# Kernel tuning notes

Hardware: AMD Instinct MI355X
Metric: run time of the kernel (lower is better)

## Reference

```python
import jax, jax.numpy as jnp
import numpy as np

D_MODEL = 2048
D_STATE = 64
D_HEAD = 64
EXPAND = 2
CHUNK = 256
D_INNER = EXPAND * D_MODEL          # 4096
N_HEADS = D_INNER // D_HEAD          # 64
PARAM_DIM = 1 + 2 * D_STATE          # 129


def setup_inputs() -> dict:
    key = jax.random.key(0)
    k0, k1, k2, k3 = jax.random.split(key, 4)
    x = jax.random.normal(k0, (1, 4096, D_MODEL), jnp.float32)
    w_in = jax.random.normal(k1, (2 * D_INNER, D_MODEL), jnp.float32) * 0.02
    w_param = jax.random.normal(k2, (N_HEADS * PARAM_DIM, D_MODEL), jnp.float32) * 0.02
    w_out = jax.random.normal(k3, (D_MODEL, D_INNER), jnp.float32) * 0.02
    return {"x": x, "w_in": w_in, "w_param": w_param, "w_out": w_out}


def _ssd(a, Bm, Cm, X, Q):
    # a: (nb, l), Bm/Cm: (nb, l, ds), X: (nb, l, dh). Mamba-2 SSD chunked scan.
    nb, l = a.shape
    ds = Bm.shape[-1]
    dh = X.shape[-1]
    nc = l // Q
    la = jnp.log(a).reshape(nb, nc, Q)
    cs = jnp.cumsum(la, axis=-1)                      # cumulative log-decay within chunk
    Bc = Bm.reshape(nb, nc, Q, ds)
    Cc = Cm.reshape(nb, nc, Q, ds)
    Xc = X.reshape(nb, nc, Q, dh)
    # intra-chunk (attention-like dual): L[i,j] = prod_{r=j+1..i} a_r, j<=i
    tri = jnp.tril(jnp.ones((Q, Q), bool))
    L = jnp.where(tri, jnp.exp(cs[..., :, None] - cs[..., None, :]), 0.0)
    scores = jnp.einsum('znid,znjd->znij', Cc, Bc) * L
    y_diag = jnp.einsum('znij,znjh->znih', scores, Xc)
    # per-chunk state contribution: sum_j decay_to_end[j] * B_j^T x_j -> (nb,nc,ds,dh)
    decay_states = jnp.exp(cs[..., -1:] - cs)
    states = jnp.einsum('znj,znjd,znjh->zndh', decay_states, Bc, Xc)
    A_chunk = jnp.exp(cs[..., -1])                    # total decay per chunk (nb, nc)
    def step(S, inp):
        Ac, st = inp
        S_prev = S
        return Ac[:, None, None] * S + st, S_prev
    S0 = jnp.zeros((nb, ds, dh), a.dtype)
    _, S_prev = jax.lax.scan(step, S0, (A_chunk.T, jnp.moveaxis(states, 1, 0)))
    S_prev = jnp.moveaxis(S_prev, 0, 1)               # state entering each chunk (nb,nc,ds,dh)
    y_inter = jnp.einsum('znid,zndh,zni->znih', Cc, S_prev, jnp.exp(cs))
    return (y_diag + y_inter).reshape(nb, l, dh)


def reference(x, w_in, w_param, w_out):
    b, l, _ = x.shape
    xr = x @ w_in.T                                   # (b, l, 2*d_inner)
    inp, res = xr[..., :D_INNER], xr[..., D_INNER:]
    params = (x @ w_param.T).reshape(b, l, N_HEADS, PARAM_DIM)
    dt = jax.nn.softplus(params[..., 0])
    a = jnp.exp(-dt)                                  # (b, l, n_heads)
    Bp = params[..., 1:1 + D_STATE]
    Cp = params[..., 1 + D_STATE:]
    nb = b * N_HEADS
    # NOTE: raw row-major reshapes, mirroring the torch source exactly
    y = _ssd(a.reshape(nb, l),
             Bp.reshape(nb, l, D_STATE),
             Cp.reshape(nb, l, D_STATE),
             inp.reshape(nb, l, D_HEAD),
             CHUNK)
    y = y.reshape(b, l, D_INNER)
    out = y * jax.nn.silu(res)
    return out @ w_out.T
```

## Files before the change

kernel.cpp:

```cpp
#include <hip/hip_runtime.h>
#include <math.h>

#define Q 256

typedef unsigned short u16;
typedef unsigned int u32;
typedef __attribute__((ext_vector_type(8))) short short8;
typedef __attribute__((ext_vector_type(4))) float f32x4;

__device__ __forceinline__ float bf2f(u32 u){
  union { float f; u32 i; } v; v.i = u << 16; return v.f;
}
__device__ __forceinline__ u16 f2bf(float f){
  union { float f; u32 i; } v; v.f = f;
  u32 r = (v.i + 0x7FFFu + ((v.i >> 16) & 1u)) >> 16;
  return (u16)r;
}
__device__ __forceinline__ float softplusf(float x){
  return x > 20.f ? x : log1pf(expf(x));
}
__device__ __forceinline__ float siluf(float x){
  return x / (1.f + expf(-x));
}

__device__ __forceinline__ void gload_lds16(const void* g, const void* l){
  __builtin_amdgcn_global_load_lds(
    (const __attribute__((address_space(1))) void*)(uintptr_t)g,
    (__attribute__((address_space(3))) void*)(u32)(uintptr_t)l,
    16, 0, 0);
}

__device__ __forceinline__ u32 swz_off(int row, int col2){
  return (u32)(row*128 + (col2 ^ ((row & 7) << 4)));
}
__device__ __forceinline__ short8 frag_ld(const u16* buf, int row, int kk, int lk){
  return *(const short8*)((const char*)buf + row*128 + (((kk*4 + lk) ^ (row & 7)) << 4));
}

__global__ __launch_bounds__(256) void cast_all(const float* __restrict__ x,
    const float* __restrict__ w_in, const float* __restrict__ w_param,
    const float* __restrict__ w_out, u16* __restrict__ xb,
    u16* __restrict__ w_in_b, u16* __restrict__ w_param_b, u16* __restrict__ w_out_b)
{
  const size_t g = (size_t)blockIdx.x * 256 + threadIdx.x;
  const float* src; u16* dst; size_t off;
  if (g < 2097152)        { src = x;       dst = xb;        off = g; }
  else if (g < 6291456)   { src = w_in;    dst = w_in_b;    off = g - 2097152; }
  else if (g < 10518528)  { src = w_param; dst = w_param_b; off = g - 6291456; }
  else                    { src = w_out;   dst = w_out_b;   off = g - 10518528; }
  const float4 v = *(const float4*)(src + off*4);
  ushort4 o;
  o.x = f2bf(v.x); o.y = f2bf(v.y); o.z = f2bf(v.z); o.w = f2bf(v.w);
  *(ushort4*)(dst + off*4) = o;
}

#define T256_STAGE(s_) \
  _Pragma("unroll") for (int q = 0; q < 3; q++) \
    gload_lds16(sptr[q] + (s_)*32, lds + (((s_)&1)*24576) + (q*512 + tid)*16);

#define T256_CORE(A_, B_, K_, NTN_) \
  __shared__ char lds[49152]; \
  const int tid = threadIdx.x; \
  const int nwg = gridDim.x, bid = blockIdx.x; \
  const int wg = (bid & 7) * (nwg >> 3) + (bid >> 3); \
  const int m0 = (wg / (NTN_)) * 128, n0 = (wg % (NTN_)) * 256; \
  const int w = tid >> 6, l = tid & 63; \
  const int wr = w >> 2, wc = w & 3; \
  const int lr = l & 15, lk = l >> 4; \
  const u16* sptr[3]; \
  _Pragma("unroll") for (int q = 0; q < 3; q++) { \
    const int c = q*512 + tid; \
    const int r = c >> 3; \
    const int lg = (c & 7) ^ (r & 7); \
    const int lrow2 = 2*r + (lg >> 2); \
    const int kc = lg & 3; \
    sptr[q] = (lrow2 < 128) ? ((A_) + (size_t)(m0 + lrow2)*(K_) + kc*8) \
                            : ((B_) + (size_t)(n0 + (lrow2 - 128))*(K_) + kc*8); \
  } \
  const int arow0 = wr*64 + lr; \
  const int abrow = arow0 >> 1; \
  const int abase = abrow*128 + ((((arow0 & 1)*4 + lk) ^ (abrow & 7)) << 4); \
  const int brow0 = 64 + ((wc*64 + lr) >> 1); \
  const int bbase = brow0*128 + ((((lr & 1)*4 + lk) ^ (brow0 & 7)) << 4); \
  f32x4 acc[4][4]; \
  { f32x4 z = {0.f,0.f,0.f,0.f}; \
    _Pragma("unroll") for (int m = 0; m < 4; m++) \
    _Pragma("unroll") for (int n = 0; n < 4; n++) acc[m][n] = z; } \
  T256_STAGE(0) \
  asm volatile("s_waitcnt vmcnt(0)" ::: "memory"); \
  __builtin_amdgcn_s_barrier(); \
  { const int NS = (K_)/32; \
    for (int s = 0; s < NS-1; ++s) { \
      const char* sb_ = lds + ((s & 1)*24576); \
      short8 aF[4], bF[4]; \
      T256_STAGE(s+1) \
      _Pragma("unroll") for (int m = 0; m < 4; m++) \
        aF[m] = *(const short8*)(sb_ + abase + m*1024); \
      _Pragma("unroll") for (int n = 0; n < 4; n++) \
        bF[n] = *(const short8*)(sb_ + bbase + n*1024); \
      __builtin_amdgcn_s_setprio(1); \
      _Pragma("unroll") for (int m = 0; m < 4; m++) \
      _Pragma("unroll") for (int n = 0; n < 4; n++) \
        acc[m][n] = __builtin_amdgcn_mfma_f32_16x16x32_bf16(aF[m], bF[n], acc[m][n], 0, 0, 0); \
      __builtin_amdgcn_s_setprio(0); \
      asm volatile("s_waitcnt vmcnt(0)" ::: "memory"); \
      __builtin_amdgcn_s_barrier(); \
    } \
    { const char* sb_ = lds + (((K_)/32 - 1) & 1)*24576; \
      short8 aF[4], bF[4]; \
      _Pragma("unroll") for (int m = 0; m < 4; m++) \
        aF[m] = *(const short8*)(sb_ + abase + m*1024); \
      _Pragma("unroll") for (int n = 0; n < 4; n++) \
        bF[n] = *(const short8*)(sb_ + bbase + n*1024); \
      _Pragma("unroll") for (int m = 0; m < 4; m++) \
      _Pragma("unroll") for (int n = 0; n < 4; n++) \
        acc[m][n] = __builtin_amdgcn_mfma_f32_16x16x32_bf16(aF[m], bF[n], acc[m][n], 0, 0, 0); \
    } \
  }

__global__ void __launch_bounds__(512, 4) gemm_in256(const u16* __restrict__ A,
    const u16* __restrict__ B, u16* __restrict__ inp, u16* __restrict__ resb)
{
  T256_CORE(A, B, 2048, 32)
  #pragma unroll
  for (int m = 0; m < 4; m++)
    #pragma unroll
    for (int n = 0; n < 4; n++) {
      const int col = n0 + wc*64 + n*16 + lr;
      #pragma unroll
      for (int j = 0; j < 4; j++) {
        const int row = m0 + wr*64 + m*16 + lk*4 + j;
        const u16 v = f2bf(acc[m][n][j]);
        if (col < 4096) inp[(size_t)row*4096 + col] = v;
        else            resb[(size_t)row*4096 + (col - 4096)] = v;
      }
    }
}

__global__ void __launch_bounds__(512, 4) gemm_par256(const u16* __restrict__ A,
    const u16* __restrict__ B, float* __restrict__ dtb,
    u16* __restrict__ Bb, u16* __restrict__ Cb)
{
  T256_CORE(A, B, 2048, 33)
  #pragma unroll
  for (int m = 0; m < 4; m++)
    #pragma unroll
    for (int n = 0; n < 4; n++) {
      const int col = n0 + wc*64 + n*16 + lr;
      if (col < 8256) {
        const int h = col / 129, rr = col - h*129;
        #pragma unroll
        for (int j = 0; j < 4; j++) {
          const int row = m0 + wr*64 + m*16 + lk*4 + j;
          const float v = acc[m][n][j];
          if (rr == 0)      dtb[(size_t)row*64 + h] = v;
          else if (rr < 65) Bb[((size_t)row*64 + h)*64 + (rr-1)]  = f2bf(v);
          else              Cb[((size_t)row*64 + h)*64 + (rr-65)] = f2bf(v);
        }
      }
    }
}

__global__ void __launch_bounds__(512, 4) gemm_out256(const u16* __restrict__ A,
    const u16* __restrict__ B, float* __restrict__ C)
{
  T256_CORE(A, B, 4096, 8)
  #pragma unroll
  for (int m = 0; m < 4; m++)
    #pragma unroll
    for (int n = 0; n < 4; n++) {
      const int col = n0 + wc*64 + n*16 + lr;
      #pragma unroll
      for (int j = 0; j < 4; j++)
        C[(size_t)(m0 + wr*64 + m*16 + lk*4 + j)*2048 + col] = acc[m][n][j];
    }
}

__global__ __launch_bounds__(256) void ssd_phaseA(const float* __restrict__ dtb,
    const u16* __restrict__ Bb, const u16* __restrict__ inp,
    float* __restrict__ cs_g, float* __restrict__ achunk, float* __restrict__ states_t)
{
  const int g = blockIdx.x, tid = threadIdx.x;
  const int p = g * Q + tid;
  __shared__ float sc[Q];
  __shared__ u16 sBt[64*64];
  __shared__ u16 sXt[64*64];
  sc[tid] = -softplusf(dtb[p]);
  __syncthreads();
  for (int off = 1; off < Q; off <<= 1) {
    float v = (tid >= off) ? sc[tid - off] : 0.f;
    __syncthreads();
    if (tid >= off) sc[tid] += v;
    __syncthreads();
  }
  cs_g[p] = sc[tid];
  const float cl = sc[Q-1];
  if (tid == 0) achunk[g] = expf(cl);

  const int w = tid >> 6, l = tid & 63;
  const int lrow = l & 15, lk = l >> 4;
  const int tj = tid & 63, tcb = (tid >> 6) * 16;
  f32x4 acc[4];
  { f32x4 z = {0,0,0,0}; acc[0]=z; acc[1]=z; acc[2]=z; acc[3]=z; }

  for (int js = 0; js < 4; js++) {
    __syncthreads();
    {
      const int jc = js*64 + tj;
      const float wj = expf(cl - sc[jc]);
      const size_t prow = ((size_t)g*Q + jc) * 64;
      union { uint4 v; u16 s[8]; } b0, b1, x0, x1;
      b0.v = *(const uint4*)&Bb[prow + tcb];
      b1.v = *(const uint4*)&Bb[prow + tcb + 8];
      x0.v = *(const uint4*)&inp[prow + tcb];
      x1.v = *(const uint4*)&inp[prow + tcb + 8];
      #pragma unroll
      for (int q = 0; q < 8; q++) {
        const int r0 = tcb + q, r1 = tcb + 8 + q;
        *(u16*)((char*)sBt + swz_off(r0, 2*tj)) = f2bf(wj * bf2f((u32)b0.s[q]));
        *(u16*)((char*)sBt + swz_off(r1, 2*tj)) = f2bf(wj * bf2f((u32)b1.s[q]));
        *(u16*)((char*)sXt + swz_off(r0, 2*tj)) = x0.s[q];
        *(u16*)((char*)sXt + swz_off(r1, 2*tj)) = x1.s[q];
      }
    }
    __syncthreads();
    short8 aX0 = frag_ld(sXt, w*16 + lrow, 0, lk);
    short8 aX1 = frag_ld(sXt, w*16 + lrow, 1, lk);
    #pragma unroll
    for (int n = 0; n < 4; n++) {
      short8 b0 = frag_ld(sBt, n*16 + lrow, 0, lk);
      short8 b1 = frag_ld(sBt, n*16 + lrow, 1, lk);
      acc[n] = __builtin_amdgcn_mfma_f32_16x16x32_bf16(aX0, b0, acc[n], 0, 0, 0);
      acc[n] = __builtin_amdgcn_mfma_f32_16x16x32_bf16(aX1, b1, acc[n], 0, 0, 0);
    }
  }
  #pragma unroll
  for (int reg = 0; reg < 4; reg++) {
    const int d = w*16 + lk*4 + reg;
    #pragma unroll
    for (int n = 0; n < 4; n++)
      states_t[(size_t)g*4096 + d*64 + n*16 + lrow] = acc[n][reg];
  }
}

__global__ __launch_bounds__(256) void ssd_scan(float* __restrict__ states,
    const float* __restrict__ achunk)
{
  const int n = blockIdx.x, tid = threadIdx.x;
  float S[16];
  #pragma unroll
  for (int k = 0; k < 16; k++) S[k] = 0.f;
  for (int c = 0; c < 16; c++) {
    const int g = n*16 + c;
    const float A = achunk[g];
    #pragma unroll
    for (int k = 0; k < 16; k++) {
      const size_t e = (size_t)g * 4096 + tid + k*256;
      const float st = states[e];
      states[e] = S[k];
      S[k] = fmaf(A, S[k], st);
    }
  }
}

__global__ __launch_bounds__(256) void ssd_diag(const u16* __restrict__ Bb,
    const u16* __restrict__ Cb, const u16* __restrict__ inp,
    const float* __restrict__ cs_g, const float* __restrict__ states_t,
    const u16* __restrict__ resb, u16* __restrict__ yb)
{
  const int g = blockIdx.y, it = blockIdx.x, tid = threadIdx.x;
  const int w = tid >> 6, l = tid & 63;
  const int lrow = l & 15, lk = l >> 4;
  const int p_base = g * Q;
  __shared__ u16 sC[64*64];
  __shared__ u16 sB[64*64];
  __shared__ u16 sX[64*64];
  __shared__ u16 sP[64*64];
  __shared__ float csi[64], csj[64];

  const int r = tid >> 2, c0 = (tid & 3) << 4;
  {
    const size_t prow = (size_t)(p_base + it*64 + r) * 64;
    uint4 v0 = *(const uint4*)&Cb[prow + c0];
    uint4 v1 = *(const uint4*)&Cb[prow + c0 + 8];
    *(uint4*)((char*)sC + swz_off(r, c0*2))      = v0;
    *(uint4*)((char*)sC + swz_off(r, c0*2 + 16)) = v1;
    if (tid < 64) csi[tid] = cs_g[p_base + it*64 + tid];
  }
  const int i0 = w * 16;
  const int xj = tid & 63, xdb = (tid >> 6) * 16;
  f32x4 accY[4];
  { f32x4 z = {0,0,0,0}; accY[0]=z; accY[1]=z; accY[2]=z; accY[3]=z; }

  for (int jt = 0; jt <= it; jt++) {
    __syncthreads();
    {
      const size_t prow = (size_t)(p_base + jt*64 + r) * 64;
      uint4 v0 = *(const uint4*)&Bb[prow + c0];
      uint4 v1 = *(const uint4*)&Bb[prow + c0 + 8];
      *(uint4*)((char*)sB + swz_off(r, c0*2))      = v0;
      *(uint4*)((char*)sB + swz_off(r, c0*2 + 16)) = v1;
      if (tid < 64) csj[tid] = cs_g[p_base + jt*64 + tid];
    }
    {
      const size_t prow = (size_t)(p_base + jt*64 + xj) * 64;
      union { uint4 v; u16 s[8]; } x0, x1;
      x0.v = *(const uint4*)&inp[prow + xdb];
      x1.v = *(const uint4*)&inp[prow + xdb + 8];
      #pragma unroll
      for (int q = 0; q < 8; q++) {
        *(u16*)((char*)sX + swz_off(xdb + q,     2*xj)) = x0.s[q];
        *(u16*)((char*)sX + swz_off(xdb + 8 + q, 2*xj)) = x1.s[q];
      }
    }
    __syncthreads();
    f32x4 sAcc[4];
    { f32x4 z = {0,0,0,0}; sAcc[0]=z; sAcc[1]=z; sAcc[2]=z; sAcc[3]=z; }
    {
      short8 aC0 = frag_ld(sC, i0 + lrow, 0, lk);
      short8 aC1 = frag_ld(sC, i0 + lrow, 1, lk);
      #pragma unroll
      for (int n = 0; n < 4; n++) {
        short8 b0 = frag_ld(sB, n*16 + lrow, 0, lk);
        short8 b1 = frag_ld(sB, n*16 + lrow, 1, lk);
        sAcc[n] = __builtin_amdgcn_mfma_f32_16x16x32_bf16(aC0, b0, sAcc[n], 0, 0, 0);
        sAcc[n] = __builtin_amdgcn_mfma_f32_16x16x32_bf16(aC1, b1, sAcc[n], 0, 0, 0);
      }
    }
    const bool full = (jt < it);
    #pragma unroll
    for (int n = 0; n < 4; n++) {
      const int j_l = n*16 + lrow;
      const float cj = csj[j_l];
      #pragma unroll
      for (int reg = 0; reg < 4; reg++) {
        const int i_l = i0 + lk*4 + reg;
        float s = 0.f;
        if (full || j_l <= i_l) s = sAcc[n][reg] * expf(csi[i_l] - cj);
        *(u16*)((char*)sP + swz_off(i_l, n*32 + 2*lrow)) = f2bf(s);
      }
    }
    {
      short8 aP0 = frag_ld(sP, i0 + lrow, 0, lk);
      short8 aP1 = frag_ld(sP, i0 + lrow, 1, lk);
      #pragma unroll
      for (int n = 0; n < 4; n++) {
        short8 x0f = frag_ld(sX, n*16 + lrow, 0, lk);
        short8 x1f = frag_ld(sX, n*16 + lrow, 1, lk);
        accY[n] = __builtin_amdgcn_mfma_f32_16x16x32_bf16(aP0, x0f, accY[n], 0, 0, 0);
        accY[n] = __builtin_amdgcn_mfma_f32_16x16x32_bf16(aP1, x1f, accY[n], 0, 0, 0);
      }
    }
  }
  __syncthreads();
  {
    const int d = tid & 63, sb = (tid >> 6) * 16;
    const float* srow = &states_t[(size_t)g*4096 + d*64 + sb];
    float4 f0 = *(const float4*)(srow);
    float4 f1 = *(const float4*)(srow + 4);
    float4 f2 = *(const float4*)(srow + 8);
    float4 f3 = *(const float4*)(srow + 12);
    union { uint4 v; u16 s[8]; } o0, o1;
    o0.s[0]=f2bf(f0.x); o0.s[1]=f2bf(f0.y); o0.s[2]=f2bf(f0.z); o0.s[3]=f2bf(f0.w);
    o0.s[4]=f2bf(f1.x); o0.s[5]=f2bf(f1.y); o0.s[6]=f2bf(f1.z); o0.s[7]=f2bf(f1.w);
    o1.s[0]=f2bf(f2.x); o1.s[1]=f2bf(f2.y); o1.s[2]=f2bf(f2.z); o1.s[3]=f2bf(f2.w);
    o1.s[4]=f2bf(f3.x); o1.s[5]=f2bf(f3.y); o1.s[6]=f2bf(f3.z); o1.s[7]=f2bf(f3.w);
    *(uint4*)((char*)sB + swz_off(d, sb*2))      = o0.v;
    *(uint4*)((char*)sB + swz_off(d, sb*2 + 16)) = o1.v;
  }
  __syncthreads();
  f32x4 accI[4];
  { f32x4 z = {0,0,0,0}; accI[0]=z; accI[1]=z; accI[2]=z; accI[3]=z; }
  {
    short8 aC0 = frag_ld(sC, i0 + lrow, 0, lk);
    short8 aC1 = frag_ld(sC, i0 + lrow, 1, lk);
    #pragma unroll
    for (int n = 0; n < 4; n++) {
      short8 s0 = frag_ld(sB, n*16 + lrow, 0, lk);
      short8 s1 = frag_ld(sB, n*16 + lrow, 1, lk);
      accI[n] = __builtin_amdgcn_mfma_f32_16x16x32_bf16(aC0, s0, accI[n], 0, 0, 0);
      accI[n] = __builtin_amdgcn_mfma_f32_16x16x32_bf16(aC1, s1, accI[n], 0, 0, 0);
    }
  }
  #pragma unroll
  for (int reg = 0; reg < 4; reg++) {
    const int i_l = i0 + lk*4 + reg;
    const float ei = expf(csi[i_l]);
    const size_t prow = (size_t)(p_base + it*64 + i_l) * 64;
    #pragma unroll
    for (int n = 0; n < 4; n++) {
      const int d = n*16 + lrow;
      const float yv = accY[n][reg] + ei * accI[n][reg];
      const float rv = bf2f((u32)resb[prow + d]);
      yb[prow + d] = f2bf(yv * siluf(rv));
    }
  }
}

extern "C" void kernel_launch(void* const* d_in, const int* in_sizes, int n_in,
                              void* d_out, int out_size, void* d_ws, size_t ws_size,
                              hipStream_t stream)
{
  const float* x       = (const float*)d_in[0];
  const float* w_in    = (const float*)d_in[1];
  const float* w_param = (const float*)d_in[2];
  const float* w_out   = (const float*)d_in[3];
  float* out = (float*)d_out;
  char* ws = (char*)d_ws;

  float* states    = (float*)(ws);
  u16*   xb        = (u16*)  (ws);
  u16*   yb        = (u16*)  (ws + 0x1000000ull);
  u16*   w_in_b    = (u16*)  (ws + 0x1000000ull);
  u16*   w_param_b = (u16*)  (ws + 0x3000000ull);
  u16*   w_out_b   = (u16*)  (ws + 0x5100000ull);
  u16*   inp       = (u16*)  (ws + 0x6100000ull);
  u16*   resb      = (u16*)  (ws + 0x8100000ull);
  u16*   Bb        = (u16*)  (ws + 0xA100000ull);
  u16*   Cb        = (u16*)  (ws + 0xC100000ull);
  float* dtb       = (float*)(ws + 0xE100000ull);
  float* cs        = (float*)(ws + 0xE200000ull);
  float* achunk    = (float*)(ws + 0xE300000ull);

  cast_all<<<49280, 256, 0, stream>>>(x, w_in, w_param, w_out,
                                      xb, w_in_b, w_param_b, w_out_b);

  gemm_in256 <<<1024, 512, 0, stream>>>(xb, w_in_b, inp, resb);
  gemm_par256<<<1056, 512, 0, stream>>>(xb, w_param_b, dtb, Bb, Cb);
  ssd_phaseA<<<1024, 256, 0, stream>>>(dtb, Bb, inp, cs, achunk, states);
  ssd_scan<<<64, 256, 0, stream>>>(states, achunk);
  ssd_diag<<<dim3(4, 1024), 256, 0, stream>>>(Bb, Cb, inp, cs, states, resb, yb);
  gemm_out256<<<256, 512, 0, stream>>>(yb, w_out_b, out);
}
```

Measured before the change: 561.9 us.

## Merge input and param GEMMs into one launch; retile output GEMM to 128x128

The input and parameter projection GEMMs now share one grid, and each workgroup selects its weight matrix and epilogue by index. This removes a launch boundary and the tail idle time between the two kernels. The output GEMM uses 128x128 tiles with a 64-deep K step, doubling the workgroup count to fill more CUs. The smaller tiles reuse less data per load, and the larger LDS footprint can lower occupancy.

```diff
diff --git a/kernel.cpp b/kernel.cpp
--- a/kernel.cpp
+++ b/kernel.cpp
@@ -58,12 +58,8 @@
   _Pragma("unroll") for (int q = 0; q < 3; q++) \
     gload_lds16(sptr[q] + (s_)*32, lds + (((s_)&1)*24576) + (q*512 + tid)*16);
 
-#define T256_CORE(A_, B_, K_, NTN_) \
+#define T256_BODY(A_, B_, K_) \
   __shared__ char lds[49152]; \
-  const int tid = threadIdx.x; \
-  const int nwg = gridDim.x, bid = blockIdx.x; \
-  const int wg = (bid & 7) * (nwg >> 3) + (bid >> 3); \
-  const int m0 = (wg / (NTN_)) * 128, n0 = (wg % (NTN_)) * 256; \
   const int w = tid >> 6, l = tid & 63; \
   const int wr = w >> 2, wc = w & 3; \
   const int lr = l & 15, lk = l >> 4; \
@@ -118,58 +114,145 @@
     } \
   }
 
-__global__ void __launch_bounds__(512, 4) gemm_in256(const u16* __restrict__ A,
-    const u16* __restrict__ B, u16* __restrict__ inp, u16* __restrict__ resb)
-{
-  T256_CORE(A, B, 2048, 32)
-  #pragma unroll
-  for (int m = 0; m < 4; m++)
-    #pragma unroll
-    for (int n = 0; n < 4; n++) {
-      const int col = n0 + wc*64 + n*16 + lr;
-      #pragma unroll
-      for (int j = 0; j < 4; j++) {
-        const int row = m0 + wr*64 + m*16 + lk*4 + j;
-        const u16 v = f2bf(acc[m][n][j]);
-        if (col < 4096) inp[(size_t)row*4096 + col] = v;
-        else            resb[(size_t)row*4096 + (col - 4096)] = v;
-      }
-    }
-}
-
-__global__ void __launch_bounds__(512, 4) gemm_par256(const u16* __restrict__ A,
-    const u16* __restrict__ B, float* __restrict__ dtb,
-    u16* __restrict__ Bb, u16* __restrict__ Cb)
-{
-  T256_CORE(A, B, 2048, 33)
-  #pragma unroll
-  for (int m = 0; m < 4; m++)
-    #pragma unroll
-    for (int n = 0; n < 4; n++) {
-      const int col = n0 + wc*64 + n*16 + lr;
-      if (col < 8256) {
-        const int h = col / 129, rr = col - h*129;
+__global__ void __launch_bounds__(512, 4) gemm_inpar(const u16* __restrict__ A,
+    const u16* __restrict__ Bin, const u16* __restrict__ Bpar,
+    u16* __restrict__ inp, u16* __restrict__ resb,
+    float* __restrict__ dtb, u16* __restrict__ Bb, u16* __restrict__ Cb)
+{
+  const int tid = threadIdx.x;
+  const int nwg = gridDim.x, bid = blockIdx.x;
+  const int wg = (bid & 7) * (nwg >> 3) + (bid >> 3);
+  const bool isPar = (wg >= 1024);
+  int m0, n0;
+  const u16* Bmat;
+  if (!isPar) { Bmat = Bin;  m0 = (wg >> 5) * 128;        n0 = (wg & 31) * 256; }
+  else        { Bmat = Bpar; const int w2 = wg - 1024;
+                m0 = (w2 / 33) * 128;                      n0 = (w2 % 33) * 256; }
+  T256_BODY(A, Bmat, 2048)
+  if (!isPar) {
+    #pragma unroll
+    for (int m = 0; m < 4; m++)
+      #pragma unroll
+      for (int n = 0; n < 4; n++) {
+        const int col = n0 + wc*64 + n*16 + lr;
         #pragma unroll
         for (int j = 0; j < 4; j++) {
           const int row = m0 + wr*64 + m*16 + lk*4 + j;
-          const float v = acc[m][n][j];
-          if (rr == 0)      dtb[(size_t)row*64 + h] = v;
-          else if (rr < 65) Bb[((size_t)row*64 + h)*64 + (rr-1)]  = f2bf(v);
-          else              Cb[((size_t)row*64 + h)*64 + (rr-65)] = f2bf(v);
+          const u16 v = f2bf(acc[m][n][j]);
+          if (col < 4096) inp[(size_t)row*4096 + col] = v;
+          else            resb[(size_t)row*4096 + (col - 4096)] = v;
         }
       }
-    }
-}
-
-__global__ void __launch_bounds__(512, 4) gemm_out256(const u16* __restrict__ A,
+  } else {
+    #pragma unroll
+    for (int m = 0; m < 4; m++)
+      #pragma unroll
+      for (int n = 0; n < 4; n++) {
+        const int col = n0 + wc*64 + n*16 + lr;
+        if (col < 8256) {
+          const int h = col / 129, rr = col - h*129;
+          #pragma unroll
+          for (int j = 0; j < 4; j++) {
+            const int row = m0 + wr*64 + m*16 + lk*4 + j;
+            const float v = acc[m][n][j];
+            if (rr == 0)      dtb[(size_t)row*64 + h] = v;
+            else if (rr < 65) Bb[((size_t)row*64 + h)*64 + (rr-1)]  = f2bf(v);
+            else              Cb[((size_t)row*64 + h)*64 + (rr-65)] = f2bf(v);
+          }
+        }
+      }
+  }
+}
+
+#define O128_STAGE(s_) \
+  _Pragma("unroll") for (int q = 0; q < 4; q++) \
+    gload_lds16(sptr[q] + (s_)*64, lds + (((s_)&1)*32768) + (q*512 + tid)*16);
+
+__global__ void __launch_bounds__(512, 4) gemm_out64(const u16* __restrict__ A,
     const u16* __restrict__ B, float* __restrict__ C)
 {
-  T256_CORE(A, B, 4096, 8)
+  __shared__ char lds[65536];
+  const int tid = threadIdx.x;
+  const int nwg = gridDim.x, bid = blockIdx.x;
+  const int wg = (bid & 7) * (nwg >> 3) + (bid >> 3);
+  const int m0 = (wg >> 4) * 128, n0 = (wg & 15) * 128;
+  const int w = tid >> 6, l = tid & 63;
+  const int wr = w >> 2, wc = w & 3;
+  const int lr = l & 15, lk = l >> 4;
+  const u16* sptr[4];
+  #pragma unroll
+  for (int q = 0; q < 4; q++) {
+    const int c = q*512 + tid;
+    const int r = c >> 3;
+    const int jl = (c & 7) ^ (r & 7);
+    sptr[q] = (r < 128) ? (A + (size_t)(m0 + r)*4096 + jl*8)
+                        : (B + (size_t)(n0 + (r - 128))*4096 + jl*8);
+  }
+  const int ko0 = ((lk       ^ (lr & 7)) << 4);
+  const int ko1 = (((4 + lk) ^ (lr & 7)) << 4);
+  const int abase = (wr*64 + lr) * 128;
+  const int bbase = (128 + wc*32 + lr) * 128;
+  f32x4 acc[4][2];
+  { f32x4 z = {0.f,0.f,0.f,0.f};
+    #pragma unroll
+    for (int m = 0; m < 4; m++)
+      #pragma unroll
+      for (int n = 0; n < 2; n++) acc[m][n] = z; }
+  O128_STAGE(0)
+  asm volatile("s_waitcnt vmcnt(0)" ::: "memory");
+  __builtin_amdgcn_s_barrier();
+  for (int s = 0; s < 63; ++s) {
+    const char* sb_ = lds + ((s & 1)*32768);
+    short8 aF[2][4], bF[2][2];
+    O128_STAGE(s+1)
+    #pragma unroll
+    for (int m = 0; m < 4; m++) {
+      aF[0][m] = *(const short8*)(sb_ + abase + m*2048 + ko0);
+      aF[1][m] = *(const short8*)(sb_ + abase + m*2048 + ko1);
+    }
+    #pragma unroll
+    for (int n = 0; n < 2; n++) {
+      bF[0][n] = *(const short8*)(sb_ + bbase + n*2048 + ko0);
+      bF[1][n] = *(const short8*)(sb_ + bbase + n*2048 + ko1);
+    }
+    __builtin_amdgcn_s_setprio(1);
+    #pragma unroll
+    for (int m = 0; m < 4; m++)
+      #pragma unroll
+      for (int n = 0; n < 2; n++)
+        #pragma unroll
+        for (int kk = 0; kk < 2; kk++)
+          acc[m][n] = __builtin_amdgcn_mfma_f32_16x16x32_bf16(aF[kk][m], bF[kk][n], acc[m][n], 0, 0, 0);
+    __builtin_amdgcn_s_setprio(0);
+    asm volatile("s_waitcnt vmcnt(0)" ::: "memory");
+    __builtin_amdgcn_s_barrier();
+  }
+  {
+    const char* sb_ = lds + ((63 & 1)*32768);
+    short8 aF[2][4], bF[2][2];
+    #pragma unroll
+    for (int m = 0; m < 4; m++) {
+      aF[0][m] = *(const short8*)(sb_ + abase + m*2048 + ko0);
+      aF[1][m] = *(const short8*)(sb_ + abase + m*2048 + ko1);
+    }
+    #pragma unroll
+    for (int n = 0; n < 2; n++) {
+      bF[0][n] = *(const short8*)(sb_ + bbase + n*2048 + ko0);
+      bF[1][n] = *(const short8*)(sb_ + bbase + n*2048 + ko1);
+    }
+    #pragma unroll
+    for (int m = 0; m < 4; m++)
+      #pragma unroll
+      for (int n = 0; n < 2; n++)
+        #pragma unroll
+        for (int kk = 0; kk < 2; kk++)
+          acc[m][n] = __builtin_amdgcn_mfma_f32_16x16x32_bf16(aF[kk][m], bF[kk][n], acc[m][n], 0, 0, 0);
+  }
   #pragma unroll
   for (int m = 0; m < 4; m++)
     #pragma unroll
-    for (int n = 0; n < 4; n++) {
-      const int col = n0 + wc*64 + n*16 + lr;
+    for (int n = 0; n < 2; n++) {
+      const int col = n0 + wc*32 + n*16 + lr;
       #pragma unroll
       for (int j = 0; j < 4; j++)
         C[(size_t)(m0 + wr*64 + m*16 + lk*4 + j)*2048 + col] = acc[m][n][j];
@@ -425,10 +508,10 @@
   cast_all<<<49280, 256, 0, stream>>>(x, w_in, w_param, w_out,
                                       xb, w_in_b, w_param_b, w_out_b);
 
-  gemm_in256 <<<1024, 512, 0, stream>>>(xb, w_in_b, inp, resb);
-  gemm_par256<<<1056, 512, 0, stream>>>(xb, w_param_b, dtb, Bb, Cb);
+  gemm_inpar<<<2080, 512, 0, stream>>>(xb, w_in_b, w_param_b,
+                                       inp, resb, dtb, Bb, Cb);
   ssd_phaseA<<<1024, 256, 0, stream>>>(dtb, Bb, inp, cs, achunk, states);
   ssd_scan<<<64, 256, 0, stream>>>(states, achunk);
   ssd_diag<<<dim3(4, 1024), 256, 0, stream>>>(Bb, Cb, inp, cs, states, resb, yb);
-  gemm_out256<<<256, 512, 0, stream>>>(yb, w_out_b, out);
-}
+  gemm_out64<<<512, 512, 0, stream>>>(yb, w_out_b, out);
+}
```

New measurement: 546.7 us (median of 2 runs). 1.03x faster.
